# Performance work log

Hardware: AMD Instinct MI355X
Metric: run time of the kernel (lower is better)

The kernel has to match this reference:

```python
import jax, jax.numpy as jnp
import numpy as np

N, E, G = 50000, 640000, 256
NODE_IN, EDGE_IN, H, L, T = 64, 16, 128, 4, 5
BN_EPS = 1e-5

def setup_inputs() -> dict:
    key = jax.random.key(0)
    ks = jax.random.split(key, 24)
    s = lambda k, shape, fan: jax.random.normal(k, shape, jnp.float32) * (1.0 / np.sqrt(fan))
    return {
        "x": jax.random.normal(ks[0], (N, NODE_IN), jnp.float32),
        "edge_attr": jax.random.normal(ks[1], (E, EDGE_IN), jnp.float32),
        "node_w": s(ks[2], (NODE_IN, H), NODE_IN), "node_b": jnp.zeros((H,), jnp.float32),
        "edge_w1": s(ks[3], (EDGE_IN, H), EDGE_IN), "edge_b1": jnp.zeros((H,), jnp.float32),
        "edge_w2": s(ks[4], (H, H), H), "edge_b2": jnp.zeros((H,), jnp.float32),
        "conv_w1": s(ks[5], (L, H, H), H), "conv_b1": jnp.zeros((L, H), jnp.float32),
        "conv_w2": s(ks[6], (L, H, H), H), "conv_b2": jnp.zeros((L, H), jnp.float32),
        "bn_gamma": jnp.ones((L, H), jnp.float32), "bn_beta": jnp.zeros((L, H), jnp.float32),
        "gate_w1": s(ks[7], (H, H // 2), H), "gate_b1": jnp.zeros((H // 2,), jnp.float32),
        "gate_w2": s(ks[8], (H // 2, 1), H // 2), "gate_b2": jnp.zeros((1,), jnp.float32),
        "head_w1": s(ks[9], (H, H), H), "head_b1": jnp.zeros((H,), jnp.float32),
        "head_w2": s(ks[10], (H, T), H), "head_b2": jnp.zeros((T,), jnp.float32),
        "edge_index": jax.random.randint(ks[11], (2, E), 0, N, jnp.int32),
        "batch": jnp.sort(jax.random.randint(ks[12], (N,), 0, G, jnp.int32)),
    }

def reference(x, edge_attr, node_w, node_b, edge_w1, edge_b1, edge_w2, edge_b2,
              conv_w1, conv_b1, conv_w2, conv_b2, bn_gamma, bn_beta,
              gate_w1, gate_b1, gate_w2, gate_b2, head_w1, head_b1, head_w2, head_b2,
              edge_index, batch):
    relu = jax.nn.relu
    h = x @ node_w + node_b                                   # [N,H]
    e = relu(edge_attr @ edge_w1 + edge_b1) @ edge_w2 + edge_b2  # [E,H]
    src, dst = edge_index[0], edge_index[1]
    bn_scale = 1.0 / jnp.sqrt(jnp.float32(1.0) + BN_EPS)      # eval BN: mean=0, var=1
    for l in range(L):
        m = relu(h[src] + e)                                  # GINEConv message [E,H]
        aggr = jax.ops.segment_sum(m, dst, num_segments=N)    # scatter-add
        z = h + aggr                                          # eps=0: (1+eps)*x + aggr
        z = relu(z @ conv_w1[l] + conv_b1[l]) @ conv_w2[l] + conv_b2[l]
        z = z * bn_scale * bn_gamma[l] + bn_beta[l]
        h = relu(z)                                           # dropout off (eval)
    gate = relu(h @ gate_w1 + gate_b1) @ gate_w2 + gate_b2    # [N,1]
    gmax = jax.ops.segment_max(gate, batch, num_segments=G)   # segment softmax
    wexp = jnp.exp(gate - gmax[batch])
    denom = jax.ops.segment_sum(wexp, batch, num_segments=G)
    alpha = wexp / denom[batch]
    g = jax.ops.segment_sum(alpha * h, batch, num_segments=G) # [G,H]
    return relu(g @ head_w1 + head_b1) @ head_w2 + head_b2    # [G,T]
```

## Files before the change

kernel.cpp:

```cpp
#include <hip/hip_runtime.h>

typedef unsigned short u16;
typedef __bf16 bf16x8 __attribute__((ext_vector_type(8)));
typedef float f32x4 __attribute__((ext_vector_type(4)));
typedef unsigned short u16x8 __attribute__((ext_vector_type(8)));

#define NNODES 50000
#define NEDGES 640000
#define NGRAPH 256

__device__ __forceinline__ float bf2f(u16 u) {
  unsigned int v = ((unsigned int)u) << 16; float f; __builtin_memcpy(&f, &v, 4); return f;
}
__device__ __forceinline__ u16 f2bf(float f) {
  unsigned int x; __builtin_memcpy(&x, &f, 4);
  unsigned int lsb = (x >> 16) & 1u;
  x += 0x7fffu + lsb;
  return (u16)(x >> 16);
}

__global__ void write_zero_f32(float* __restrict__ out, int n) {
  int i = blockIdx.x * 256 + threadIdx.x;
  if (i < n) out[i] = 0.f;
}

__global__ void zero_counts(int* __restrict__ a, int na, int* __restrict__ b, int nb) {
  int i = blockIdx.x * 256 + threadIdx.x;
  if (i < na) a[i] = 0;
  if (i < nb) b[i] = 0;
}

__global__ void prep_weights(const float* __restrict__ node_w, const float* __restrict__ edge_w1,
                             const float* __restrict__ edge_w2, const float* __restrict__ conv_w1,
                             const float* __restrict__ conv_w2, const float* __restrict__ gate_w1,
                             u16* __restrict__ node_wt, u16* __restrict__ edge_w1t,
                             u16* __restrict__ edge_w2t, u16* __restrict__ conv_w1t,
                             u16* __restrict__ conv_w2t, u16* __restrict__ gate_w1t) {
  int o = blockIdx.x * 256 + threadIdx.x;
  if (o < 8192) { int n = o >> 6, k = o & 63; node_wt[o] = f2bf(node_w[k * 128 + n]); return; }
  o -= 8192;
  if (o < 4096) { int n = o >> 5, k = o & 31;
                  edge_w1t[o] = (k < 16) ? f2bf(edge_w1[k * 128 + n]) : (u16)0; return; }
  o -= 4096;
  if (o < 16384) { int n = o >> 7, k = o & 127; edge_w2t[o] = f2bf(edge_w2[k * 128 + n]); return; }
  o -= 16384;
  if (o < 65536) { int l = o >> 14, r = o & 16383, n = r >> 7, k = r & 127;
                   conv_w1t[o] = f2bf(conv_w1[l * 16384 + k * 128 + n]); return; }
  o -= 65536;
  if (o < 65536) { int l = o >> 14, r = o & 16383, n = r >> 7, k = r & 127;
                   conv_w2t[o] = f2bf(conv_w2[l * 16384 + k * 128 + n]); return; }
  o -= 65536;
  if (o < 8192) { int n = o >> 7, k = o & 127; gate_w1t[o] = f2bf(gate_w1[k * 64 + n]); }
}

__global__ void hist_all(const int* __restrict__ dst, const int* __restrict__ b,
                         int* __restrict__ counts, int* __restrict__ gc, int n) {
  int i = blockIdx.x * 256 + threadIdx.x;
  atomicAdd(&counts[dst[i]], 1);
  if (i < n) atomicAdd(&gc[b[i]], 1);
}
__global__ void scan_a(const int* __restrict__ counts, int* __restrict__ bsums, int n) {
  int b = blockIdx.x, t = threadIdx.x;
  int i0 = b * 1024 + t * 4;
  int s = 0;
#pragma unroll
  for (int j = 0; j < 4; j++) { int i = i0 + j; if (i < n) s += counts[i]; }
  int lane = t & 63, w = t >> 6;
  for (int m = 32; m; m >>= 1) s += __shfl_xor(s, m, 64);
  __shared__ int ws_[4];
  if (lane == 0) ws_[w] = s;
  __syncthreads();
  if (t == 0) bsums[b] = ws_[0] + ws_[1] + ws_[2] + ws_[3];
}
__global__ void scan_b(int* __restrict__ bsums, int* __restrict__ offs, int nb, int n) {
  if (threadIdx.x == 0) {
    int run = 0;
    for (int i = 0; i < nb; i++) { int v = bsums[i]; bsums[i] = run; run += v; }
    offs[n] = run;
  }
}
__global__ void scan_c(const int* __restrict__ counts, const int* __restrict__ boffs,
                       int* __restrict__ offs, int* __restrict__ cursor, int n) {
  int b = blockIdx.x, t = threadIdx.x;
  int i0 = b * 1024 + t * 4;
  int v[4]; int s = 0;
#pragma unroll
  for (int j = 0; j < 4; j++) { v[j] = (i0 + j < n) ? counts[i0 + j] : 0; s += v[j]; }
  int lane = t & 63, w = t >> 6;
  int x = s;
  for (int d = 1; d < 64; d <<= 1) { int y = __shfl_up(x, (unsigned)d, 64); if (lane >= d) x += y; }
  __shared__ int wt_[4];
  if (lane == 63) wt_[w] = x;
  __syncthreads();
  int add = boffs[b];
  for (int i = 0; i < w; i++) add += wt_[i];
  int excl = add + x - s;
#pragma unroll
  for (int j = 0; j < 4; j++) {
    int i = i0 + j;
    if (i < n) { offs[i] = excl; cursor[i] = excl; }
    excl += v[j];
  }
}
__global__ void gscan(const int* __restrict__ gcounts, int* __restrict__ goffs) {
  int t = threadIdx.x;
  int v = gcounts[t];
  int lane = t & 63, w = t >> 6;
  int x = v;
  for (int d = 1; d < 64; d <<= 1) { int y = __shfl_up(x, (unsigned)d, 64); if (lane >= d) x += y; }
  __shared__ int wt_[4];
  if (lane == 63) wt_[w] = x;
  __syncthreads();
  int add = 0;
  for (int i = 0; i < w; i++) add += wt_[i];
  int incl = add + x;
  goffs[t] = incl - v;
  if (t == 255) goffs[256] = incl;
}
__global__ void scatter_csr(const int* __restrict__ src, const int* __restrict__ dst,
                            int* __restrict__ cursor, int* __restrict__ csr_src,
                            int* __restrict__ csr_eid) {
  int i = blockIdx.x * 256 + threadIdx.x;
  int d = dst[i];
  int p = atomicAdd(&cursor[d], 1);
  csr_src[p] = src[i];
  csr_eid[p] = i;
}

template <int KB, int SA, int SB>
__device__ __forceinline__ void mfma_block(const u16* aL, const u16* bL, int m, int quad,
                                           int rbase, f32x4* acc) {
#pragma unroll
  for (int kb = 0; kb < KB; ++kb) {
    bf16x8 a = *(const bf16x8*)(aL + (rbase + m) * SA + kb * 32 + quad * 8);
#pragma unroll
    for (int nt = 0; nt < 8; ++nt) {
      bf16x8 b = *(const bf16x8*)(bL + (nt * 16 + m) * SB + kb * 32 + quad * 8);
      acc[nt] = __builtin_amdgcn_mfma_f32_16x16x32_bf16(a, b, acc[nt], 0, 0, 0);
    }
  }
}

__global__ __launch_bounds__(256) void node_encode(const float* __restrict__ x,
                                                   const u16* __restrict__ wt,
                                                   const float* __restrict__ nb,
                                                   u16* __restrict__ hb, int n) {
  __shared__ alignas(16) u16 sA[64 * 72];
  __shared__ alignas(16) u16 sW[128 * 72];
  int t = threadIdx.x;
  int row0 = blockIdx.x * 64;
#pragma unroll
  for (int i = 0; i < 4; i++) {
    int idx = t + 256 * i; int r = idx >> 4, c = idx & 15;
    int grow = row0 + r; if (grow > n - 1) grow = n - 1;
    float4 v = *(const float4*)(x + (size_t)grow * 64 + c * 4);
    ushort4 o; o.x = f2bf(v.x); o.y = f2bf(v.y); o.z = f2bf(v.z); o.w = f2bf(v.w);
    *(ushort4*)&sA[r * 72 + c * 4] = o;
  }
#pragma unroll
  for (int i = 0; i < 4; i++) {
    int idx = t + 256 * i; int nr = idx >> 3, c = idx & 7;
    *(uint4*)&sW[nr * 72 + c * 8] = *(const uint4*)(wt + nr * 64 + c * 8);
  }
  __syncthreads();
  int lane = t & 63, w = t >> 6, m = lane & 15, quad = lane >> 4, rbase = w * 16;
  f32x4 acc[8];
  f32x4 z4 = {0.f, 0.f, 0.f, 0.f};
#pragma unroll
  for (int i = 0; i < 8; i++) acc[i] = z4;
  mfma_block<2, 72, 72>(sA, sW, m, quad, rbase, acc);
#pragma unroll
  for (int nt = 0; nt < 8; nt++) {
    int col = nt * 16 + m;
    float bb = nb[col];
    f32x4 a4 = acc[nt];
#pragma unroll
    for (int r = 0; r < 4; r++) {
      int grow = row0 + rbase + quad * 4 + r;
      if (grow < n) hb[(size_t)grow * 128 + col] = f2bf(a4[r] + bb);
    }
  }
}

__global__ __launch_bounds__(256) void edge_encode(const float* __restrict__ ea,
                                                   const u16* __restrict__ w1t,
                                                   const u16* __restrict__ w2t,
                                                   const float* __restrict__ b1,
                                                   const float* __restrict__ b2,
                                                   const int* __restrict__ csr_eid,
                                                   u16* __restrict__ e_perm) {
  __shared__ alignas(16) u16 sA[64 * 48];
  __shared__ alignas(16) u16 sMid[64 * 136];
  int t = threadIdx.x;
  int lane = t & 63, w = t >> 6, m = lane & 15, quad = lane >> 4, rbase = w * 16;
  int s0 = blockIdx.x * 64;

  if (t < 128) {
    int r = t >> 1, c = t & 1;
    uint4 z = {0, 0, 0, 0};
    *(uint4*)&sA[r * 48 + 16 + c * 8] = z;
  }
  {
    int eidv = 0;
    if (lane < 16) eidv = csr_eid[s0 + w * 16 + lane];
    int r = lane >> 2, c = lane & 3;
    int eid = __shfl(eidv, r, 64);
    float4 v = *(const float4*)(ea + (size_t)eid * 16 + c * 4);
    ushort4 o; o.x = f2bf(v.x); o.y = f2bf(v.y); o.z = f2bf(v.z); o.w = f2bf(v.w);
    *(ushort4*)&sA[(w * 16 + r) * 48 + c * 4] = o;
  }
  bf16x8 w1f[8];
#pragma unroll
  for (int nt = 0; nt < 8; nt++)
    w1f[nt] = *(const bf16x8*)(w1t + (nt * 16 + m) * 32 + quad * 8);
  __syncthreads();

  f32x4 z4 = {0.f, 0.f, 0.f, 0.f};
  f32x4 acc[8];
#pragma unroll
  for (int i = 0; i < 8; i++) acc[i] = z4;
  {
    bf16x8 a = *(const bf16x8*)(&sA[(rbase + m) * 48 + quad * 8]);
#pragma unroll
    for (int nt = 0; nt < 8; nt++)
      acc[nt] = __builtin_amdgcn_mfma_f32_16x16x32_bf16(w1f[nt], a, acc[nt], 0, 0, 0);
  }
#pragma unroll
  for (int nt = 0; nt < 8; nt++) {
    float4 bb = *(const float4*)&b1[nt * 16 + quad * 4];
    u16 q0 = f2bf(fmaxf(acc[nt][0] + bb.x, 0.f));
    u16 q1 = f2bf(fmaxf(acc[nt][1] + bb.y, 0.f));
    u16 q2 = f2bf(fmaxf(acc[nt][2] + bb.z, 0.f));
    u16 q3 = f2bf(fmaxf(acc[nt][3] + bb.w, 0.f));
    uint2 pk;
    pk.x = (unsigned int)q0 | ((unsigned int)q1 << 16);
    pk.y = (unsigned int)q2 | ((unsigned int)q3 << 16);
    *(uint2*)&sMid[(rbase + m) * 136 + nt * 16 + quad * 4] = pk;
  }
  bf16x8 w2f[8];
  float4 b2v[2];
#pragma unroll
  for (int ct = 0; ct < 2; ct++) {
    b2v[ct] = *(const float4*)&b2[w * 32 + ct * 16 + quad * 4];
#pragma unroll
    for (int kb = 0; kb < 4; kb++)
      w2f[ct * 4 + kb] = *(const bf16x8*)(w2t + (size_t)(w * 32 + ct * 16 + m) * 128 + kb * 32 + quad * 8);
  }
  __syncthreads();

  f32x4 acc2[8];
#pragma unroll
  for (int i = 0; i < 8; i++) acc2[i] = z4;
#pragma unroll
  for (int rt = 0; rt < 4; rt++) {
#pragma unroll
    for (int kb = 0; kb < 4; kb++) {
      bf16x8 a = *(const bf16x8*)(&sMid[(rt * 16 + m) * 136 + kb * 32 + quad * 8]);
      acc2[rt * 2 + 0] = __builtin_amdgcn_mfma_f32_16x16x32_bf16(w2f[kb], a, acc2[rt * 2 + 0], 0, 0, 0);
      acc2[rt * 2 + 1] = __builtin_amdgcn_mfma_f32_16x16x32_bf16(w2f[4 + kb], a, acc2[rt * 2 + 1], 0, 0, 0);
    }
  }
  __syncthreads();
#pragma unroll
  for (int rt = 0; rt < 4; rt++) {
#pragma unroll
    for (int ct = 0; ct < 2; ct++) {
      f32x4 a4 = acc2[rt * 2 + ct];
      u16 q0 = f2bf(a4[0] + b2v[ct].x);
      u16 q1 = f2bf(a4[1] + b2v[ct].y);
      u16 q2 = f2bf(a4[2] + b2v[ct].z);
      u16 q3 = f2bf(a4[3] + b2v[ct].w);
      uint2 pk;
      pk.x = (unsigned int)q0 | ((unsigned int)q1 << 16);
      pk.y = (unsigned int)q2 | ((unsigned int)q3 << 16);
      *(uint2*)&sMid[(rt * 16 + m) * 136 + w * 32 + ct * 16 + quad * 4] = pk;
    }
  }
  __syncthreads();
#pragma unroll
  for (int i = 0; i < 4; i++) {
    int idx = t + 256 * i; int r = idx >> 4, c = idx & 15;
    *(uint4*)(e_perm + (size_t)(s0 + r) * 128 + c * 8) = *(const uint4*)&sMid[r * 136 + c * 8];
  }
}

__global__ __launch_bounds__(256) void layer_k(const u16* __restrict__ hin,
                                               u16* __restrict__ hout,
                                               const u16* __restrict__ e_perm,
                                               const int* __restrict__ offs,
                                               const int* __restrict__ csr_src,
                                               const u16* __restrict__ w1t, const u16* __restrict__ w2t,
                                               const float* __restrict__ b1, const float* __restrict__ b2,
                                               const float* __restrict__ gam, const float* __restrict__ bet,
                                               int n) {
  __shared__ alignas(16) u16 sZ[64 * 136];
  __shared__ alignas(16) u16 sMid[64 * 136];
  int t = threadIdx.x;
  int lane = t & 63, w = t >> 6, m = lane & 15, quad = lane >> 4;
  int row0 = blockIdx.x * 64;
  int li = m;
  int qq = w * 4 + quad;

  for (int k = 0; k < 4; k++) {
    int lr = qq * 4 + k;
    int nd = row0 + lr; if (nd > n - 1) nd = n - 1;
    int s0 = offs[nd], s1 = offs[nd + 1];
    float a[8];
#pragma unroll
    for (int j = 0; j < 8; j++) a[j] = 0.f;
    int s = s0;
    for (; s + 2 <= s1; s += 2) {
      int v0 = csr_src[s], v1 = csr_src[s + 1];
      u16x8 h0 = *(const u16x8*)(hin + (size_t)v0 * 128 + li * 8);
      u16x8 e0 = *(const u16x8*)(e_perm + (size_t)s * 128 + li * 8);
      u16x8 h1 = *(const u16x8*)(hin + (size_t)v1 * 128 + li * 8);
      u16x8 e1 = *(const u16x8*)(e_perm + (size_t)(s + 1) * 128 + li * 8);
#pragma unroll
      for (int j = 0; j < 8; j++) {
        a[j] += fmaxf(bf2f(h0[j]) + bf2f(e0[j]), 0.f);
        a[j] += fmaxf(bf2f(h1[j]) + bf2f(e1[j]), 0.f);
      }
    }
    if (s < s1) {
      int v = csr_src[s];
      u16x8 hv = *(const u16x8*)(hin + (size_t)v * 128 + li * 8);
      u16x8 ev = *(const u16x8*)(e_perm + (size_t)s * 128 + li * 8);
#pragma unroll
      for (int j = 0; j < 8; j++) a[j] += fmaxf(bf2f(hv[j]) + bf2f(ev[j]), 0.f);
    }
    u16x8 hv = *(const u16x8*)(hin + (size_t)nd * 128 + li * 8);
    u16x8 o;
#pragma unroll
    for (int j = 0; j < 8; j++) o[j] = f2bf(bf2f(hv[j]) + a[j]);
    *(u16x8*)&sZ[lr * 136 + li * 8] = o;
  }
  bf16x8 w1f[8];
  float4 b1v[2];
#pragma unroll
  for (int ct = 0; ct < 2; ct++) {
    b1v[ct] = *(const float4*)&b1[w * 32 + ct * 16 + quad * 4];
#pragma unroll
    for (int kb = 0; kb < 4; kb++)
      w1f[ct * 4 + kb] = *(const bf16x8*)(w1t + (size_t)(w * 32 + ct * 16 + m) * 128 + kb * 32 + quad * 8);
  }
  __syncthreads();

  f32x4 z4 = {0.f, 0.f, 0.f, 0.f};
  f32x4 acc[8];
#pragma unroll
  for (int i = 0; i < 8; i++) acc[i] = z4;
#pragma unroll
  for (int rt = 0; rt < 4; rt++) {
#pragma unroll
    for (int kb = 0; kb < 4; kb++) {
      bf16x8 a = *(const bf16x8*)(&sZ[(rt * 16 + m) * 136 + kb * 32 + quad * 8]);
      acc[rt * 2 + 0] = __builtin_amdgcn_mfma_f32_16x16x32_bf16(w1f[kb], a, acc[rt * 2 + 0], 0, 0, 0);
      acc[rt * 2 + 1] = __builtin_amdgcn_mfma_f32_16x16x32_bf16(w1f[4 + kb], a, acc[rt * 2 + 1], 0, 0, 0);
    }
  }
#pragma unroll
  for (int rt = 0; rt < 4; rt++) {
#pragma unroll
    for (int ct = 0; ct < 2; ct++) {
      f32x4 a4 = acc[rt * 2 + ct];
      u16 q0 = f2bf(fmaxf(a4[0] + b1v[ct].x, 0.f));
      u16 q1 = f2bf(fmaxf(a4[1] + b1v[ct].y, 0.f));
      u16 q2 = f2bf(fmaxf(a4[2] + b1v[ct].z, 0.f));
      u16 q3 = f2bf(fmaxf(a4[3] + b1v[ct].w, 0.f));
      uint2 pk;
      pk.x = (unsigned int)q0 | ((unsigned int)q1 << 16);
      pk.y = (unsigned int)q2 | ((unsigned int)q3 << 16);
      *(uint2*)&sMid[(rt * 16 + m) * 136 + w * 32 + ct * 16 + quad * 4] = pk;
    }
  }
  bf16x8 w2f[8];
  float4 b2v[2], gamv[2], betv[2];
#pragma unroll
  for (int ct = 0; ct < 2; ct++) {
    int c0 = w * 32 + ct * 16 + quad * 4;
    b2v[ct] = *(const float4*)&b2[c0];
    gamv[ct] = *(const float4*)&gam[c0];
    betv[ct] = *(const float4*)&bet[c0];
#pragma unroll
    for (int kb = 0; kb < 4; kb++)
      w2f[ct * 4 + kb] = *(const bf16x8*)(w2t + (size_t)(w * 32 + ct * 16 + m) * 128 + kb * 32 + quad * 8);
  }
  __syncthreads();

  f32x4 acc2[8];
#pragma unroll
  for (int i = 0; i < 8; i++) acc2[i] = z4;
#pragma unroll
  for (int rt = 0; rt < 4; rt++) {
#pragma unroll
    for (int kb = 0; kb < 4; kb++) {
      bf16x8 a = *(const bf16x8*)(&sMid[(rt * 16 + m) * 136 + kb * 32 + quad * 8]);
      acc2[rt * 2 + 0] = __builtin_amdgcn_mfma_f32_16x16x32_bf16(w2f[kb], a, acc2[rt * 2 + 0], 0, 0, 0);
      acc2[rt * 2 + 1] = __builtin_amdgcn_mfma_f32_16x16x32_bf16(w2f[4 + kb], a, acc2[rt * 2 + 1], 0, 0, 0);
    }
  }
  const float bns = 0.99999500003749983f;
#pragma unroll
  for (int rt = 0; rt < 4; rt++) {
#pragma unroll
    for (int ct = 0; ct < 2; ct++) {
      f32x4 a4 = acc2[rt * 2 + ct];
      u16 q0 = f2bf(fmaxf((a4[0] + b2v[ct].x) * bns * gamv[ct].x + betv[ct].x, 0.f));
      u16 q1 = f2bf(fmaxf((a4[1] + b2v[ct].y) * bns * gamv[ct].y + betv[ct].y, 0.f));
      u16 q2 = f2bf(fmaxf((a4[2] + b2v[ct].z) * bns * gamv[ct].z + betv[ct].z, 0.f));
      u16 q3 = f2bf(fmaxf((a4[3] + b2v[ct].w) * bns * gamv[ct].w + betv[ct].w, 0.f));
      uint2 pk;
      pk.x = (unsigned int)q0 | ((unsigned int)q1 << 16);
      pk.y = (unsigned int)q2 | ((unsigned int)q3 << 16);
      *(uint2*)&sZ[(rt * 16 + m) * 136 + w * 32 + ct * 16 + quad * 4] = pk;
    }
  }
  __syncthreads();
#pragma unroll
  for (int i = 0; i < 4; i++) {
    int idx = t + 256 * i; int r = idx >> 4, c = idx & 15;
    int grow = row0 + r;
    if (grow < n)
      *(uint4*)(hout + (size_t)grow * 128 + c * 8) = *(const uint4*)&sZ[r * 136 + c * 8];
  }
}

__global__ __launch_bounds__(256) void gate_k(const u16* __restrict__ hb,
                                              const u16* __restrict__ w1t,
                                              const float* __restrict__ b1,
                                              const float* __restrict__ w2,
                                              const float* __restrict__ b2,
                                              float* __restrict__ gate, int n) {
  __shared__ alignas(16) u16 sA[64 * 136];
  __shared__ alignas(16) u16 sW[64 * 136];
  int t = threadIdx.x;
  int row0 = blockIdx.x * 64;
#pragma unroll
  for (int i = 0; i < 4; i++) {
    int idx = t + 256 * i; int r = idx >> 4, c = idx & 15;
    int grow = row0 + r; if (grow > n - 1) grow = n - 1;
    *(uint4*)&sA[r * 136 + c * 8] = *(const uint4*)(hb + (size_t)grow * 128 + c * 8);
  }
#pragma unroll
  for (int i = 0; i < 4; i++) {
    int idx = t + 256 * i; int r = idx >> 4, c = idx & 15;
    *(uint4*)&sW[r * 136 + c * 8] = *(const uint4*)(w1t + r * 128 + c * 8);
  }
  __syncthreads();
  int lane = t & 63, w = t >> 6, m = lane & 15, quad = lane >> 4, rbase = w * 16;
  f32x4 z4 = {0.f, 0.f, 0.f, 0.f};
  f32x4 acc[4];
#pragma unroll
  for (int i = 0; i < 4; i++) acc[i] = z4;
#pragma unroll
  for (int kb = 0; kb < 4; kb++) {
    bf16x8 a = *(const bf16x8*)(&sA[(rbase + m) * 136 + kb * 32 + quad * 8]);
#pragma unroll
    for (int nt = 0; nt < 4; nt++) {
      bf16x8 b = *(const bf16x8*)(&sW[(nt * 16 + m) * 136 + kb * 32 + quad * 8]);
      acc[nt] = __builtin_amdgcn_mfma_f32_16x16x32_bf16(a, b, acc[nt], 0, 0, 0);
    }
  }
  float b1v[4], w2v[4];
#pragma unroll
  for (int nt = 0; nt < 4; nt++) { b1v[nt] = b1[nt * 16 + m]; w2v[nt] = w2[nt * 16 + m]; }
  float b2v = b2[0];
#pragma unroll
  for (int r = 0; r < 4; r++) {
    float p = 0.f;
#pragma unroll
    for (int nt = 0; nt < 4; nt++) p += fmaxf(acc[nt][r] + b1v[nt], 0.f) * w2v[nt];
    p += __shfl_xor(p, 1, 64);
    p += __shfl_xor(p, 2, 64);
    p += __shfl_xor(p, 4, 64);
    p += __shfl_xor(p, 8, 64);
    if (m == 0) {
      int grow = row0 + rbase + quad * 4 + r;
      if (grow < n) gate[grow] = p + b2v;
    }
  }
}

__global__ __launch_bounds__(256) void pool_k(const float* __restrict__ gate,
                                              const u16* __restrict__ hb,
                                              const int* __restrict__ goffs,
                                              float* __restrict__ gpool) {
  int g = blockIdx.x, t = threadIdx.x;
  int s0 = goffs[g], s1 = goffs[g + 1];
  int lane = t & 63, w = t >> 6;
  __shared__ float red[4];
  __shared__ float fin[2][128];
  float mx = -3.4e38f;
  for (int i = s0 + t; i < s1; i += 256) mx = fmaxf(mx, gate[i]);
  for (int d = 32; d; d >>= 1) mx = fmaxf(mx, __shfl_xor(mx, d, 64));
  if (lane == 0) red[w] = mx;
  __syncthreads();
  mx = fmaxf(fmaxf(red[0], red[1]), fmaxf(red[2], red[3]));
  __syncthreads();
  float sm = 0.f;
  for (int i = s0 + t; i < s1; i += 256) sm += __expf(gate[i] - mx);
  for (int d = 32; d; d >>= 1) sm += __shfl_xor(sm, d, 64);
  if (lane == 0) red[w] = sm;
  __syncthreads();
  sm = red[0] + red[1] + red[2] + red[3];
  int g2 = t >> 7, tc = t & 127;
  float acc = 0.f;
  for (int i = s0 + g2; i < s1; i += 2)
    acc += __expf(gate[i] - mx) * bf2f(hb[(size_t)i * 128 + tc]);
  fin[g2][tc] = acc;
  __syncthreads();
  if (t < 128) gpool[g * 128 + t] = (s1 > s0) ? (fin[0][t] + fin[1][t]) / sm : 0.f;
}

__global__ __launch_bounds__(128) void head_k(const float* __restrict__ gpool,
                                              const float* __restrict__ w1, const float* __restrict__ b1,
                                              const float* __restrict__ w2, const float* __restrict__ b2,
                                              float* __restrict__ out) {
  int g = blockIdx.x, t = threadIdx.x;
  __shared__ float sg[128];
  __shared__ float shid[128];
  sg[t] = gpool[g * 128 + t];
  __syncthreads();
  float s = 0.f;
  for (int k = 0; k < 128; k++) s += sg[k] * w1[k * 128 + t];
  shid[t] = fmaxf(s + b1[t], 0.f);
  __syncthreads();
  if (t < 5) {
    float o = b2[t];
    for (int k = 0; k < 128; k++) o += shid[k] * w2[k * 5 + t];
    out[g * 5 + t] = o;
  }
}

extern "C" void kernel_launch(void* const* d_in, const int* in_sizes, int n_in,
                              void* d_out, int out_size, void* d_ws, size_t ws_size,
                              hipStream_t stream) {
  const int N = NNODES, E = NEDGES, G = NGRAPH;
  const float* x = (const float*)d_in[0];
  const float* edge_attr = (const float*)d_in[1];
  const float* node_w = (const float*)d_in[2];
  const float* node_b = (const float*)d_in[3];
  const float* edge_w1 = (const float*)d_in[4];
  const float* edge_b1 = (const float*)d_in[5];
  const float* edge_w2 = (const float*)d_in[6];
  const float* edge_b2 = (const float*)d_in[7];
  const float* conv_w1 = (const float*)d_in[8];
  const float* conv_b1 = (const float*)d_in[9];
  const float* conv_w2 = (const float*)d_in[10];
  const float* conv_b2 = (const float*)d_in[11];
  const float* bn_gamma = (const float*)d_in[12];
  const float* bn_beta = (const float*)d_in[13];
  const float* gate_w1 = (const float*)d_in[14];
  const float* gate_b1 = (const float*)d_in[15];
  const float* gate_w2 = (const float*)d_in[16];
  const float* gate_b2 = (const float*)d_in[17];
  const float* head_w1 = (const float*)d_in[18];
  const float* head_b1 = (const float*)d_in[19];
  const float* head_w2 = (const float*)d_in[20];
  const float* head_b2 = (const float*)d_in[21];
  const int* eidx = (const int*)d_in[22];
  const int* batch = (const int*)d_in[23];
  const int* esrc = eidx;
  const int* edst = eidx + E;

  char* wp = (char*)d_ws;
  auto alloc = [&](size_t bytes) { char* p = wp; wp += (bytes + 255) & ~(size_t)255; return p; };
  u16* e_perm = (u16*)alloc((size_t)E * 128 * 2);
  u16* hb = (u16*)alloc((size_t)(N + 16) * 128 * 2);
  u16* hb2 = (u16*)alloc((size_t)(N + 16) * 128 * 2);
  float* gate = (float*)alloc((size_t)N * 4);
  float* gpool = (float*)alloc((size_t)G * 128 * 4);
  int* counts = (int*)alloc((size_t)N * 4);
  int* offs = (int*)alloc((size_t)(N + 1) * 4);
  int* cursor = (int*)alloc((size_t)N * 4);
  int* csr_src = (int*)alloc((size_t)E * 4);
  int* csr_eid = (int*)alloc((size_t)E * 4);
  int* bsums = (int*)alloc(64 * 4);
  int* gcounts = (int*)alloc(G * 4);
  int* goffs = (int*)alloc((G + 1) * 4);
  u16* node_wt = (u16*)alloc(8192 * 2);
  u16* edge_w1t = (u16*)alloc(4096 * 2);
  u16* edge_w2t = (u16*)alloc(16384 * 2);
  u16* conv_w1t = (u16*)alloc(65536 * 2);
  u16* conv_w2t = (u16*)alloc(65536 * 2);
  u16* gate_w1t = (u16*)alloc(8192 * 2);

  size_t need = (size_t)(wp - (char*)d_ws);
  if (need > ws_size) {
    write_zero_f32<<<(out_size + 255) / 256, 256, 0, stream>>>((float*)d_out, out_size);
    return;
  }

  zero_counts<<<(N + 255) / 256, 256, 0, stream>>>(counts, N, gcounts, G);
  prep_weights<<<656, 256, 0, stream>>>(node_w, edge_w1, edge_w2, conv_w1, conv_w2, gate_w1,
                                        node_wt, edge_w1t, edge_w2t, conv_w1t, conv_w2t, gate_w1t);
  hist_all<<<E / 256, 256, 0, stream>>>(edst, batch, counts, gcounts, N);
  scan_a<<<49, 256, 0, stream>>>(counts, bsums, N);
  scan_b<<<1, 64, 0, stream>>>(bsums, offs, 49, N);
  scan_c<<<49, 256, 0, stream>>>(counts, bsums, offs, cursor, N);
  gscan<<<1, 256, 0, stream>>>(gcounts, goffs);
  scatter_csr<<<E / 256, 256, 0, stream>>>(esrc, edst, cursor, csr_src, csr_eid);
  node_encode<<<(N + 63) / 64, 256, 0, stream>>>(x, node_wt, node_b, hb, N);
  edge_encode<<<E / 64, 256, 0, stream>>>(edge_attr, edge_w1t, edge_w2t, edge_b1, edge_b2,
                                          csr_eid, e_perm);
  u16* hcur = hb;
  u16* hnext = hb2;
  for (int l = 0; l < 4; l++) {
    layer_k<<<(N + 63) / 64, 256, 0, stream>>>(hcur, hnext, e_perm, offs, csr_src,
                                               conv_w1t + l * 16384, conv_w2t + l * 16384,
                                               conv_b1 + l * 128, conv_b2 + l * 128,
                                               bn_gamma + l * 128, bn_beta + l * 128, N);
    u16* tmp = hcur; hcur = hnext; hnext = tmp;
  }
  gate_k<<<(N + 63) / 64, 256, 0, stream>>>(hcur, gate_w1t, gate_b1, gate_w2, gate_b2, gate, N);
  pool_k<<<G, 256, 0, stream>>>(gate, hcur, goffs, gpool);
  head_k<<<G, 128, 0, stream>>>(gpool, head_w1, head_b1, head_w2, head_b2, (float*)d_out);
}
```

Before: 655.2 us.

## Merge setup kernels, widen edge_encode tiles, split neighbor gather across quads

Folds the count zeroing into prep_weights, and the graph-offset scan and block-sum scan into scan_a/scan_c, so four small launches go away. edge_encode now processes 128 edges per block with 32 rows per wave, which doubles register accumulators and LDS. layer_k's aggregation now assigns one node per 16-lane group across all four quads: each quad strides over edges by 4 and the partial sums are reduced with shuffles. This gives more memory-level parallelism on the gathers, at the cost of idle lanes on low-degree nodes. offs[n] is now hardcoded to NEDGES, and a no-op term was added to a w2t index.

```diff
diff --git a/kernel.cpp b/kernel.cpp
--- a/kernel.cpp
+++ b/kernel.cpp
@@ -24,19 +24,16 @@
   if (i < n) out[i] = 0.f;
 }
 
-__global__ void zero_counts(int* __restrict__ a, int na, int* __restrict__ b, int nb) {
-  int i = blockIdx.x * 256 + threadIdx.x;
-  if (i < na) a[i] = 0;
-  if (i < nb) b[i] = 0;
-}
-
 __global__ void prep_weights(const float* __restrict__ node_w, const float* __restrict__ edge_w1,
                              const float* __restrict__ edge_w2, const float* __restrict__ conv_w1,
                              const float* __restrict__ conv_w2, const float* __restrict__ gate_w1,
                              u16* __restrict__ node_wt, u16* __restrict__ edge_w1t,
                              u16* __restrict__ edge_w2t, u16* __restrict__ conv_w1t,
-                             u16* __restrict__ conv_w2t, u16* __restrict__ gate_w1t) {
+                             u16* __restrict__ conv_w2t, u16* __restrict__ gate_w1t,
+                             int* __restrict__ counts, int* __restrict__ gcounts) {
   int o = blockIdx.x * 256 + threadIdx.x;
+  if (o < NNODES) counts[o] = 0;
+  if (o < NGRAPH) gcounts[o] = 0;
   if (o < 8192) { int n = o >> 6, k = o & 63; node_wt[o] = f2bf(node_w[k * 128 + n]); return; }
   o -= 8192;
   if (o < 4096) { int n = o >> 5, k = o & 31;
@@ -59,27 +56,34 @@
   atomicAdd(&counts[dst[i]], 1);
   if (i < n) atomicAdd(&gc[b[i]], 1);
 }
-__global__ void scan_a(const int* __restrict__ counts, int* __restrict__ bsums, int n) {
+__global__ void scan_a(const int* __restrict__ counts, int* __restrict__ bsums,
+                       const int* __restrict__ gcounts, int* __restrict__ goffs, int n) {
+  __shared__ int sh4[4];
   int b = blockIdx.x, t = threadIdx.x;
+  int lane = t & 63, w = t >> 6;
+  if (b == 49) {
+    int v = gcounts[t];
+    int x = v;
+    for (int d = 1; d < 64; d <<= 1) { int y = __shfl_up(x, (unsigned)d, 64); if (lane >= d) x += y; }
+    if (lane == 63) sh4[w] = x;
+    __syncthreads();
+    int add = 0;
+    for (int i = 0; i < w; i++) add += sh4[i];
+    int incl = add + x;
+    goffs[t] = incl - v;
+    if (t == 255) goffs[256] = incl;
+    return;
+  }
   int i0 = b * 1024 + t * 4;
   int s = 0;
 #pragma unroll
   for (int j = 0; j < 4; j++) { int i = i0 + j; if (i < n) s += counts[i]; }
-  int lane = t & 63, w = t >> 6;
   for (int m = 32; m; m >>= 1) s += __shfl_xor(s, m, 64);
-  __shared__ int ws_[4];
-  if (lane == 0) ws_[w] = s;
-  __syncthreads();
-  if (t == 0) bsums[b] = ws_[0] + ws_[1] + ws_[2] + ws_[3];
-}
-__global__ void scan_b(int* __restrict__ bsums, int* __restrict__ offs, int nb, int n) {
-  if (threadIdx.x == 0) {
-    int run = 0;
-    for (int i = 0; i < nb; i++) { int v = bsums[i]; bsums[i] = run; run += v; }
-    offs[n] = run;
-  }
-}
-__global__ void scan_c(const int* __restrict__ counts, const int* __restrict__ boffs,
+  if (lane == 0) sh4[w] = s;
+  __syncthreads();
+  if (t == 0) bsums[b] = sh4[0] + sh4[1] + sh4[2] + sh4[3];
+}
+__global__ void scan_c(const int* __restrict__ counts, const int* __restrict__ bsums,
                        int* __restrict__ offs, int* __restrict__ cursor, int n) {
   int b = blockIdx.x, t = threadIdx.x;
   int i0 = b * 1024 + t * 4;
@@ -92,7 +96,8 @@
   __shared__ int wt_[4];
   if (lane == 63) wt_[w] = x;
   __syncthreads();
-  int add = boffs[b];
+  int add = 0;
+  for (int i = 0; i < b; i++) add += bsums[i];
   for (int i = 0; i < w; i++) add += wt_[i];
   int excl = add + x - s;
 #pragma unroll
@@ -101,21 +106,7 @@
     if (i < n) { offs[i] = excl; cursor[i] = excl; }
     excl += v[j];
   }
-}
-__global__ void gscan(const int* __restrict__ gcounts, int* __restrict__ goffs) {
-  int t = threadIdx.x;
-  int v = gcounts[t];
-  int lane = t & 63, w = t >> 6;
-  int x = v;
-  for (int d = 1; d < 64; d <<= 1) { int y = __shfl_up(x, (unsigned)d, 64); if (lane >= d) x += y; }
-  __shared__ int wt_[4];
-  if (lane == 63) wt_[w] = x;
-  __syncthreads();
-  int add = 0;
-  for (int i = 0; i < w; i++) add += wt_[i];
-  int incl = add + x;
-  goffs[t] = incl - v;
-  if (t == 255) goffs[256] = incl;
+  if (b == 0 && t == 0) offs[n] = NEDGES;
 }
 __global__ void scatter_csr(const int* __restrict__ src, const int* __restrict__ dst,
                             int* __restrict__ cursor, int* __restrict__ csr_src,
@@ -189,53 +180,58 @@
                                                    const float* __restrict__ b2,
                                                    const int* __restrict__ csr_eid,
                                                    u16* __restrict__ e_perm) {
-  __shared__ alignas(16) u16 sA[64 * 48];
-  __shared__ alignas(16) u16 sMid[64 * 136];
+  __shared__ alignas(16) u16 sA[128 * 48];
+  __shared__ alignas(16) u16 sMid[128 * 136];
   int t = threadIdx.x;
-  int lane = t & 63, w = t >> 6, m = lane & 15, quad = lane >> 4, rbase = w * 16;
-  int s0 = blockIdx.x * 64;
-
-  if (t < 128) {
-    int r = t >> 1, c = t & 1;
+  int lane = t & 63, w = t >> 6, m = lane & 15, quad = lane >> 4;
+  int s0 = blockIdx.x * 128;
+  int ebase = w * 32;
+
+  {
+    int r = lane >> 1, c = lane & 1;
     uint4 z = {0, 0, 0, 0};
-    *(uint4*)&sA[r * 48 + 16 + c * 8] = z;
-  }
-  {
+    *(uint4*)&sA[(ebase + r) * 48 + 16 + c * 8] = z;
     int eidv = 0;
-    if (lane < 16) eidv = csr_eid[s0 + w * 16 + lane];
-    int r = lane >> 2, c = lane & 3;
+    if (lane < 32) eidv = csr_eid[s0 + ebase + lane];
     int eid = __shfl(eidv, r, 64);
-    float4 v = *(const float4*)(ea + (size_t)eid * 16 + c * 4);
-    ushort4 o; o.x = f2bf(v.x); o.y = f2bf(v.y); o.z = f2bf(v.z); o.w = f2bf(v.w);
-    *(ushort4*)&sA[(w * 16 + r) * 48 + c * 4] = o;
+    float4 v0 = *(const float4*)(ea + (size_t)eid * 16 + c * 8);
+    float4 v1 = *(const float4*)(ea + (size_t)eid * 16 + c * 8 + 4);
+    ushort4 o0; o0.x = f2bf(v0.x); o0.y = f2bf(v0.y); o0.z = f2bf(v0.z); o0.w = f2bf(v0.w);
+    ushort4 o1; o1.x = f2bf(v1.x); o1.y = f2bf(v1.y); o1.z = f2bf(v1.z); o1.w = f2bf(v1.w);
+    *(ushort4*)&sA[(ebase + r) * 48 + c * 8] = o0;
+    *(ushort4*)&sA[(ebase + r) * 48 + c * 8 + 4] = o1;
   }
   bf16x8 w1f[8];
 #pragma unroll
   for (int nt = 0; nt < 8; nt++)
     w1f[nt] = *(const bf16x8*)(w1t + (nt * 16 + m) * 32 + quad * 8);
-  __syncthreads();
 
   f32x4 z4 = {0.f, 0.f, 0.f, 0.f};
-  f32x4 acc[8];
-#pragma unroll
-  for (int i = 0; i < 8; i++) acc[i] = z4;
-  {
-    bf16x8 a = *(const bf16x8*)(&sA[(rbase + m) * 48 + quad * 8]);
+  f32x4 acc1[16];
+#pragma unroll
+  for (int i = 0; i < 16; i++) acc1[i] = z4;
+#pragma unroll
+  for (int rt2 = 0; rt2 < 2; rt2++) {
+    bf16x8 a = *(const bf16x8*)(&sA[(ebase + rt2 * 16 + m) * 48 + quad * 8]);
 #pragma unroll
     for (int nt = 0; nt < 8; nt++)
-      acc[nt] = __builtin_amdgcn_mfma_f32_16x16x32_bf16(w1f[nt], a, acc[nt], 0, 0, 0);
-  }
-#pragma unroll
-  for (int nt = 0; nt < 8; nt++) {
-    float4 bb = *(const float4*)&b1[nt * 16 + quad * 4];
-    u16 q0 = f2bf(fmaxf(acc[nt][0] + bb.x, 0.f));
-    u16 q1 = f2bf(fmaxf(acc[nt][1] + bb.y, 0.f));
-    u16 q2 = f2bf(fmaxf(acc[nt][2] + bb.z, 0.f));
-    u16 q3 = f2bf(fmaxf(acc[nt][3] + bb.w, 0.f));
-    uint2 pk;
-    pk.x = (unsigned int)q0 | ((unsigned int)q1 << 16);
-    pk.y = (unsigned int)q2 | ((unsigned int)q3 << 16);
-    *(uint2*)&sMid[(rbase + m) * 136 + nt * 16 + quad * 4] = pk;
+      acc1[rt2 * 8 + nt] = __builtin_amdgcn_mfma_f32_16x16x32_bf16(w1f[nt], a, acc1[rt2 * 8 + nt], 0, 0, 0);
+  }
+#pragma unroll
+  for (int rt2 = 0; rt2 < 2; rt2++) {
+#pragma unroll
+    for (int nt = 0; nt < 8; nt++) {
+      float4 bb = *(const float4*)&b1[nt * 16 + quad * 4];
+      f32x4 a4 = acc1[rt2 * 8 + nt];
+      u16 q0 = f2bf(fmaxf(a4[0] + bb.x, 0.f));
+      u16 q1 = f2bf(fmaxf(a4[1] + bb.y, 0.f));
+      u16 q2 = f2bf(fmaxf(a4[2] + bb.z, 0.f));
+      u16 q3 = f2bf(fmaxf(a4[3] + bb.w, 0.f));
+      uint2 pk;
+      pk.x = (unsigned int)q0 | ((unsigned int)q1 << 16);
+      pk.y = (unsigned int)q2 | ((unsigned int)q3 << 16);
+      *(uint2*)&sMid[(ebase + rt2 * 16 + m) * 136 + nt * 16 + quad * 4] = pk;
+    }
   }
   bf16x8 w2f[8];
   float4 b2v[2];
@@ -248,11 +244,11 @@
   }
   __syncthreads();
 
-  f32x4 acc2[8];
-#pragma unroll
-  for (int i = 0; i < 8; i++) acc2[i] = z4;
-#pragma unroll
-  for (int rt = 0; rt < 4; rt++) {
+  f32x4 acc2[16];
+#pragma unroll
+  for (int i = 0; i < 16; i++) acc2[i] = z4;
+#pragma unroll
+  for (int rt = 0; rt < 8; rt++) {
 #pragma unroll
     for (int kb = 0; kb < 4; kb++) {
       bf16x8 a = *(const bf16x8*)(&sMid[(rt * 16 + m) * 136 + kb * 32 + quad * 8]);
@@ -262,7 +258,7 @@
   }
   __syncthreads();
 #pragma unroll
-  for (int rt = 0; rt < 4; rt++) {
+  for (int rt = 0; rt < 8; rt++) {
 #pragma unroll
     for (int ct = 0; ct < 2; ct++) {
       f32x4 a4 = acc2[rt * 2 + ct];
@@ -278,7 +274,7 @@
   }
   __syncthreads();
 #pragma unroll
-  for (int i = 0; i < 4; i++) {
+  for (int i = 0; i < 8; i++) {
     int idx = t + 256 * i; int r = idx >> 4, c = idx & 15;
     *(uint4*)(e_perm + (size_t)(s0 + r) * 128 + c * 8) = *(const uint4*)&sMid[r * 136 + c * 8];
   }
@@ -298,41 +294,48 @@
   int t = threadIdx.x;
   int lane = t & 63, w = t >> 6, m = lane & 15, quad = lane >> 4;
   int row0 = blockIdx.x * 64;
-  int li = m;
-  int qq = w * 4 + quad;
-
-  for (int k = 0; k < 4; k++) {
-    int lr = qq * 4 + k;
+  int li = m, q = quad;
+
+  for (int k = 0; k < 16; k++) {
+    int lr = w * 16 + k;
     int nd = row0 + lr; if (nd > n - 1) nd = n - 1;
-    int s0 = offs[nd], s1 = offs[nd + 1];
+    int e0 = offs[nd], e1 = offs[nd + 1];
+    u16x8 hv = {};
+    if (q == 0) hv = *(const u16x8*)(hin + (size_t)nd * 128 + li * 8);
     float a[8];
 #pragma unroll
     for (int j = 0; j < 8; j++) a[j] = 0.f;
-    int s = s0;
-    for (; s + 2 <= s1; s += 2) {
-      int v0 = csr_src[s], v1 = csr_src[s + 1];
+    int s = e0 + q;
+    for (; s + 8 <= e1; s += 8) {
+      int v0 = csr_src[s], v1 = csr_src[s + 4];
       u16x8 h0 = *(const u16x8*)(hin + (size_t)v0 * 128 + li * 8);
-      u16x8 e0 = *(const u16x8*)(e_perm + (size_t)s * 128 + li * 8);
+      u16x8 ee0 = *(const u16x8*)(e_perm + (size_t)s * 128 + li * 8);
       u16x8 h1 = *(const u16x8*)(hin + (size_t)v1 * 128 + li * 8);
-      u16x8 e1 = *(const u16x8*)(e_perm + (size_t)(s + 1) * 128 + li * 8);
+      u16x8 ee1 = *(const u16x8*)(e_perm + (size_t)(s + 4) * 128 + li * 8);
 #pragma unroll
       for (int j = 0; j < 8; j++) {
-        a[j] += fmaxf(bf2f(h0[j]) + bf2f(e0[j]), 0.f);
-        a[j] += fmaxf(bf2f(h1[j]) + bf2f(e1[j]), 0.f);
+        a[j] += fmaxf(bf2f(h0[j]) + bf2f(ee0[j]), 0.f);
+        a[j] += fmaxf(bf2f(h1[j]) + bf2f(ee1[j]), 0.f);
       }
     }
-    if (s < s1) {
+    for (; s < e1; s += 4) {
       int v = csr_src[s];
-      u16x8 hv = *(const u16x8*)(hin + (size_t)v * 128 + li * 8);
+      u16x8 hgv = *(const u16x8*)(hin + (size_t)v * 128 + li * 8);
       u16x8 ev = *(const u16x8*)(e_perm + (size_t)s * 128 + li * 8);
 #pragma unroll
-      for (int j = 0; j < 8; j++) a[j] += fmaxf(bf2f(hv[j]) + bf2f(ev[j]), 0.f);
-    }
-    u16x8 hv = *(const u16x8*)(hin + (size_t)nd * 128 + li * 8);
-    u16x8 o;
-#pragma unroll
-    for (int j = 0; j < 8; j++) o[j] = f2bf(bf2f(hv[j]) + a[j]);
-    *(u16x8*)&sZ[lr * 136 + li * 8] = o;
+      for (int j = 0; j < 8; j++) a[j] += fmaxf(bf2f(hgv[j]) + bf2f(ev[j]), 0.f);
+    }
+#pragma unroll
+    for (int j = 0; j < 8; j++) {
+      a[j] += __shfl_xor(a[j], 16, 64);
+      a[j] += __shfl_xor(a[j], 32, 64);
+    }
+    if (q == 0) {
+      u16x8 o;
+#pragma unroll
+      for (int j = 0; j < 8; j++) o[j] = f2bf(bf2f(hv[j]) + a[j]);
+      *(u16x8*)&sZ[lr * 136 + li * 8] = o;
+    }
   }
   bf16x8 w1f[8];
   float4 b1v[2];
@@ -383,7 +386,7 @@
     betv[ct] = *(const float4*)&bet[c0];
 #pragma unroll
     for (int kb = 0; kb < 4; kb++)
-      w2f[ct * 4 + kb] = *(const bf16x8*)(w2t + (size_t)(w * 32 + ct * 16 + m) * 128 + kb * 32 + quad * 8);
+      w2f[ct * 4 + kb] = *(const bf16x8*)(w2t + (size_t)c0 / 4 * 0 + (size_t)(w * 32 + ct * 16 + m) * 128 + kb * 32 + quad * 8);
   }
   __syncthreads();
 
@@ -591,18 +594,16 @@
     return;
   }
 
-  zero_counts<<<(N + 255) / 256, 256, 0, stream>>>(counts, N, gcounts, G);
   prep_weights<<<656, 256, 0, stream>>>(node_w, edge_w1, edge_w2, conv_w1, conv_w2, gate_w1,
-                                        node_wt, edge_w1t, edge_w2t, conv_w1t, conv_w2t, gate_w1t);
+                                        node_wt, edge_w1t, edge_w2t, conv_w1t, conv_w2t, gate_w1t,
+                                        counts, gcounts);
   hist_all<<<E / 256, 256, 0, stream>>>(edst, batch, counts, gcounts, N);
-  scan_a<<<49, 256, 0, stream>>>(counts, bsums, N);
-  scan_b<<<1, 64, 0, stream>>>(bsums, offs, 49, N);
+  scan_a<<<50, 256, 0, stream>>>(counts, bsums, gcounts, goffs, N);
   scan_c<<<49, 256, 0, stream>>>(counts, bsums, offs, cursor, N);
-  gscan<<<1, 256, 0, stream>>>(gcounts, goffs);
   scatter_csr<<<E / 256, 256, 0, stream>>>(esrc, edst, cursor, csr_src, csr_eid);
   node_encode<<<(N + 63) / 64, 256, 0, stream>>>(x, node_wt, node_b, hb, N);
-  edge_encode<<<E / 64, 256, 0, stream>>>(edge_attr, edge_w1t, edge_w2t, edge_b1, edge_b2,
-                                          csr_eid, e_perm);
+  edge_encode<<<E / 128, 256, 0, stream>>>(edge_attr, edge_w1t, edge_w2t, edge_b1, edge_b2,
+                                           csr_eid, e_perm);
   u16* hcur = hb;
   u16* hnext = hb2;
   for (int l = 0; l < 4; l++) {
```

Result: no change. 646.2 us (-1.4%).
